# Optimization experiments

Hardware: AMD Instinct MI355X
Metric: run time of the kernel (lower is better)

Reference implementation:

```python
import jax, jax.numpy as jnp
import numpy as np

B, D, H, W = 32, 256, 32, 32
K = 1024
BETA = 0.25


def setup_inputs() -> dict:
    key = jax.random.key(0)
    k1, k2 = jax.random.split(key)
    z_e = jax.random.normal(k1, (B, D, H, W), dtype=jnp.float32)
    codebook_weight = jax.random.normal(k2, (K, D), dtype=jnp.float32)
    return {"z_e": z_e, "codebook_weight": codebook_weight}


def reference(z_e, codebook_weight):
    # NCHW -> NHWC, flatten to tokens [N, D]
    z_perm = jnp.transpose(z_e, (0, 2, 3, 1))            # [B, H, W, D]
    z_flat = z_perm.reshape(-1, codebook_weight.shape[1])  # [N, D]

    # Squared Euclidean distances (argmin-equivalent to torch.cdist argmin)
    # d2[n, k] = ||z_n||^2 - 2 z_n . c_k + ||c_k||^2
    d2 = (jnp.sum(z_flat * z_flat, axis=1, keepdims=True)
          - 2.0 * (z_flat @ codebook_weight.T)
          + jnp.sum(codebook_weight * codebook_weight, axis=1)[None, :])  # [N, K]
    codebook_idx = jnp.argmin(d2, axis=1)                 # [N]

    # one-hot @ codebook == gather
    z_quant = codebook_weight[codebook_idx].reshape(z_perm.shape)  # [B,H,W,D]

    # straight-through estimator, back to NCHW
    z_q = z_perm + jax.lax.stop_gradient(z_quant - z_perm)
    z_q = jnp.transpose(z_q, (0, 3, 1, 2))                # [B, D, H, W]

    loss_codebook = jnp.mean((z_quant - jax.lax.stop_gradient(z_perm)) ** 2)
    loss_commit = jnp.mean((jax.lax.stop_gradient(z_quant) - z_perm) ** 2)
    loss_vq = loss_codebook + loss_commit * BETA

    return z_q, codebook_idx[:, None], loss_vq
```

## Files before the change

### kernel.cpp

```cpp
#include <hip/hip_runtime.h>
#include <hip/hip_bf16.h>
#include <cstdint>

#define B_ 32
#define D_ 256
#define K_ 1024
#define N_TOK 32768
#define Z_ELEMS 8388608
#define OUT_IDX_OFF Z_ELEMS
#define OUT_LOSS_OFF (Z_ELEMS + N_TOK)

#define WS_CNORM_OFF 0
#define WS_PART_OFF  4096
#define WS_CBF_OFF   8192
#define WS_TOP2_OFF  532480

#define MARGIN 1.25f

typedef __attribute__((ext_vector_type(8))) short short8v;
typedef __attribute__((ext_vector_type(4))) float f32x4;
typedef unsigned long long u64;

__device__ __forceinline__ unsigned short f2bf(float x) {
    unsigned u = __float_as_uint(x);
    return (unsigned short)((u + 0x7fffu + ((u >> 16) & 1u)) >> 16);
}
__device__ __forceinline__ unsigned packf(float f) {
    unsigned u = __float_as_uint(f);
    return (u & 0x80000000u) ? ~u : (u | 0x80000000u);
}
__device__ __forceinline__ float unpackf(unsigned p) {
    unsigned u = (p & 0x80000000u) ? (p & 0x7fffffffu) : ~p;
    return __uint_as_float(u);
}
__device__ __forceinline__ void gload16(const void* g, void* l) {
    __builtin_amdgcn_global_load_lds(
        (const __attribute__((address_space(1))) unsigned int*)g,
        (__attribute__((address_space(3))) unsigned int*)l, 16, 0, 0);
}

__global__ __launch_bounds__(256)
void prep_kernel(const float* __restrict__ cb, float* __restrict__ cnorm,
                 unsigned char* __restrict__ cbf) {
    const int t = threadIdx.x;
    const int blk = blockIdx.x;
    {
        int k = blk * 64 + (t >> 2);
        int part = t & 3;
        const float4* row = reinterpret_cast<const float4*>(cb + k * D_);
        float s = 0.f;
#pragma unroll
        for (int j = 0; j < 16; ++j) {
            float4 v = row[part * 16 + j];
            s += v.x * v.x + v.y * v.y + v.z * v.z + v.w * v.w;
        }
        s += __shfl_xor(s, 1);
        s += __shfl_xor(s, 2);
        if (part == 0) cnorm[k] = s;
    }
#pragma unroll
    for (int w = 0; w < 8; ++w) {
        int g = blk * 2048 + w * 256 + t;
        int lane = g & 63, ct = (g >> 6) & 7, kc = (g >> 9) & 7, cblk = g >> 12;
        int code = cblk * 128 + ct * 16 + (lane & 15);
        int d0 = kc * 32 + (lane >> 4) * 8;
        const float* src = cb + code * 256 + d0;
        float4 a = *reinterpret_cast<const float4*>(src);
        float4 b2 = *reinterpret_cast<const float4*>(src + 4);
        uint4 pk;
        pk.x = (unsigned)f2bf(a.x) | ((unsigned)f2bf(a.y) << 16);
        pk.y = (unsigned)f2bf(a.z) | ((unsigned)f2bf(a.w) << 16);
        pk.z = (unsigned)f2bf(b2.x) | ((unsigned)f2bf(b2.y) << 16);
        pk.w = (unsigned)f2bf(b2.z) | ((unsigned)f2bf(b2.w) << 16);
        *reinterpret_cast<uint4*>(cbf + (size_t)g * 16) = pk;
    }
}

__global__ __launch_bounds__(256)
void mm_kernel(const float* __restrict__ z, const unsigned char* __restrict__ cbf,
               const float* __restrict__ cnorm, unsigned* __restrict__ top2) {
    __shared__ __align__(16) unsigned char zfB[32768];
    __shared__ __align__(16) unsigned char Abuf[16384];
    __shared__ float cns[1024];

    const int t = threadIdx.x;
    const int lane = t & 63;
    const int wv = t >> 6;
    const int blk = blockIdx.x;
    const int b = blk >> 4;
    const int hw0 = (blk & 15) << 6;
    const float* zb = z + ((size_t)b << 18) + hw0;

    {
        const unsigned char* g = cbf + (size_t)(wv * 2) * 1024 + lane * 16;
        unsigned char* l = Abuf + (wv * 2) * 1024;
        gload16(g, l);
        gload16(g + 1024, l + 1024);
    }

    for (int i = t; i < 1024; i += 256) cns[i] = cnorm[i];

    {
        const int tok = t & 63;
        const int dseg = t >> 6;
#pragma unroll
        for (int u = 0; u < 8; ++u) {
            int d0 = dseg * 64 + u * 8;
            float v[8];
#pragma unroll
            for (int j = 0; j < 8; ++j) v[j] = zb[(size_t)(d0 + j) * 1024 + tok];
            uint4 pk;
            pk.x = (unsigned)f2bf(v[0]) | ((unsigned)f2bf(v[1]) << 16);
            pk.y = (unsigned)f2bf(v[2]) | ((unsigned)f2bf(v[3]) << 16);
            pk.z = (unsigned)f2bf(v[4]) | ((unsigned)f2bf(v[5]) << 16);
            pk.w = (unsigned)f2bf(v[6]) | ((unsigned)f2bf(v[7]) << 16);
            int kc = d0 >> 5;
            *reinterpret_cast<uint4*>(zfB + (kc * 4 + (tok >> 4)) * 1024 +
                                      ((u & 3) * 16 + (tok & 15)) * 16) = pk;
        }
    }
    __syncthreads();

    const int rbase = (lane >> 4) << 2;

    for (int cblk = 0; cblk < 8; ++cblk) {
        f32x4 acc[8];
#pragma unroll
        for (int mt = 0; mt < 8; ++mt) acc[mt] = (f32x4){0.f, 0.f, 0.f, 0.f};

        for (int kc = 0; kc < 8; ++kc) {
            const int s = cblk * 8 + kc;
            if (s < 63) {
                const unsigned char* g =
                    cbf + (size_t)(s + 1) * 8192 + (wv * 2) * 1024 + lane * 16;
                unsigned char* l = Abuf + ((s + 1) & 1) * 8192 + (wv * 2) * 1024;
                gload16(g, l);
                gload16(g + 1024, l + 1024);
            }
            const unsigned char* ab = Abuf + (s & 1) * 8192 + lane * 16;
            short8v bfv = *reinterpret_cast<const short8v*>(
                zfB + (kc * 4 + wv) * 1024 + lane * 16);
#pragma unroll
            for (int mt = 0; mt < 8; ++mt) {
                short8v af = *reinterpret_cast<const short8v*>(ab + mt * 1024);
                acc[mt] = __builtin_amdgcn_mfma_f32_16x16x32_bf16(af, bfv, acc[mt], 0, 0, 0);
            }
            if (kc == 7) {
                unsigned k1 = 0xFFFFFFFFu, k2 = 0xFFFFFFFFu;
#pragma unroll
                for (int mt = 0; mt < 8; ++mt) {
#pragma unroll
                    for (int r = 0; r < 4; ++r) {
                        int code = cblk * 128 + mt * 16 + rbase + r;
                        float d2a = fmaf(-2.0f, acc[mt][r], cns[code]);
                        unsigned key = (packf(d2a) & 0xFFFFFC00u) | (unsigned)code;
                        if (key < k1) { k2 = k1; k1 = key; }
                        else if (key < k2) { k2 = key; }
                    }
                }
#pragma unroll
                for (int x = 16; x <= 32; x <<= 1) {
                    unsigned o1 = __shfl_xor(k1, x);
                    unsigned o2 = __shfl_xor(k2, x);
                    unsigned n1, n2;
                    if (k1 < o1) { n1 = k1; n2 = (k2 < o1) ? k2 : o1; }
                    else         { n1 = o1; n2 = (o2 < k1) ? o2 : k1; }
                    k1 = n1; k2 = n2;
                }
                if (lane < 16) {
                    int token = blk * 64 + wv * 16 + lane;
                    *reinterpret_cast<uint2*>(top2 + ((size_t)cblk * N_TOK + token) * 2) =
                        make_uint2(k1, k2);
                }
            }
            __syncthreads();
        }
    }
}

__global__ __launch_bounds__(256)
void refgather_kernel(const float* __restrict__ z, const float* __restrict__ cb,
                      const float* __restrict__ cnorm, const unsigned* __restrict__ top2,
                      float* __restrict__ out, float* __restrict__ partials) {
    __shared__ float zsm[32][261];
    __shared__ float crows[32][257];
    __shared__ int cand[32][16];
    __shared__ int cnt[32];
    __shared__ u64 bestk[32];
    __shared__ int sidx[32];
    __shared__ float red[256];
    __shared__ int maxc;

    const int t = threadIdx.x;
    const int bh = blockIdx.x;
    const int b = bh >> 5, h = bh & 31;
    const int n0 = b * 1024 + h * 32;
    const int w = t & 31, dg = t >> 5;

    {
        const float* zp = z + ((size_t)b << 18) + h * 32 + w;
#pragma unroll
        for (int i = 0; i < 32; ++i) {
            int d = dg * 32 + i;
            zsm[w][d] = zp[(size_t)d * 1024];
        }
    }
    if (t < 32) cnt[t] = 0;
    if (t == 0) maxc = 0;
    __syncthreads();

    const int tk = t >> 3, l8 = t & 7;
    {
        uint2 kk = *reinterpret_cast<const uint2*>(
            top2 + ((size_t)l8 * N_TOK + (n0 + tk)) * 2);
        unsigned mn = kk.x;
#pragma unroll
        for (int x = 1; x < 8; x <<= 1) {
            unsigned o = __shfl_xor(mn, x);
            if (o < mn) mn = o;
        }
        float thr = unpackf(mn & 0xFFFFFC00u) + MARGIN;
        float da = unpackf(kk.x & 0xFFFFFC00u);
        if (da <= thr) { int p = atomicAdd(&cnt[tk], 1); cand[tk][p] = (int)(kk.x & 1023u); }
        float db = unpackf(kk.y & 0xFFFFFC00u);
        if (db <= thr) { int p = atomicAdd(&cnt[tk], 1); cand[tk][p] = (int)(kk.y & 1023u); }
    }
    __syncthreads();
    if (t < 32) atomicMax(&maxc, cnt[t]);
    __syncthreads();

    const int mc = maxc;
    u64 best = ~0ull;
    for (int ci = 0; ci < mc; ++ci) {
        if (ci < cnt[tk]) {
            int k = cand[tk][ci];
            const float* crow = cb + (size_t)k * 256;
            float s = 0.f;
#pragma unroll
            for (int j = 0; j < 32; ++j) {
                int d = j * 8 + l8;
                s = fmaf(zsm[tk][d], crow[d], s);
            }
#pragma unroll
            for (int x = 1; x < 8; x <<= 1) s += __shfl_xor(s, x);
            float d2 = cnorm[k] - 2.f * s;
            u64 key = ((u64)packf(d2) << 32) | (unsigned)k;
            if (key < best) best = key;
        }
    }
    if (l8 == 0) bestk[tk] = best;
    __syncthreads();
    if (t < 32) {
        int k = (int)(bestk[t] & 1023ull);
        sidx[t] = k;
        out[OUT_IDX_OFF + n0 + t] = (float)k;
    }
    __syncthreads();
    {
        const int r = t & 31, q = t >> 5;
        const float4* src = reinterpret_cast<const float4*>(cb + (size_t)sidx[r] * 256 + q * 32);
#pragma unroll
        for (int j = 0; j < 8; ++j) {
            float4 v = src[j];
            int d = q * 32 + j * 4;
            crows[r][d] = v.x; crows[r][d + 1] = v.y;
            crows[r][d + 2] = v.z; crows[r][d + 3] = v.w;
        }
    }
    __syncthreads();
    float accl = 0.f;
    float* orow = out + ((size_t)b << 18) + h * 32 + w;
#pragma unroll
    for (int i = 0; i < 32; ++i) {
        const int d = dg * 32 + i;
        const float cv = crows[w][d];
        const float zv = zsm[w][d];
        orow[(size_t)d * 1024] = cv;
        const float df = cv - zv;
        accl += df * df;
    }
    red[t] = accl;
    __syncthreads();
    for (int s = 128; s > 0; s >>= 1) {
        if (t < s) red[t] += red[t + s];
        __syncthreads();
    }
    if (t == 0) partials[bh] = red[0];
}

__global__ __launch_bounds__(256) void loss_kernel(const float* __restrict__ partials,
                                                   float* __restrict__ out) {
    __shared__ float red[256];
    const int t = threadIdx.x;
    float s = partials[t] + partials[t + 256] + partials[t + 512] + partials[t + 768];
    red[t] = s;
    __syncthreads();
    for (int st = 128; st > 0; st >>= 1) {
        if (t < st) red[t] += red[t + st];
        __syncthreads();
    }
    if (t == 0) out[OUT_LOSS_OFF] = red[0] * (1.25f / (float)Z_ELEMS);
}

extern "C" void kernel_launch(void* const* d_in, const int* in_sizes, int n_in,
                              void* d_out, int out_size, void* d_ws, size_t ws_size,
                              hipStream_t stream) {
    const float* z = (const float*)d_in[0];
    const float* cb = (const float*)d_in[1];
    float* out = (float*)d_out;
    float* cnorm = (float*)((char*)d_ws + WS_CNORM_OFF);
    float* partials = (float*)((char*)d_ws + WS_PART_OFF);
    unsigned char* cbf = (unsigned char*)d_ws + WS_CBF_OFF;
    unsigned* top2 = (unsigned*)((char*)d_ws + WS_TOP2_OFF);

    prep_kernel<<<16, 256, 0, stream>>>(cb, cnorm, cbf);
    mm_kernel<<<512, 256, 0, stream>>>(z, cbf, cnorm, top2);
    refgather_kernel<<<1024, 256, 0, stream>>>(z, cb, cnorm, top2, out, partials);
    loss_kernel<<<1, 256, 0, stream>>>(partials, out);
}
```

Baseline: 84.75 us.

## Triple-buffer codebook tiles in mm_kernel and widen prep kernel grid

The matmul kernel moves from double-buffered to triple-buffered LDS staging of bf16 codebook tiles, prefetching two steps ahead. It replaces per-step __syncthreads with a raw s_barrier plus explicit vmcnt waits and sched barriers, and flattens the cblk/kc loops into one macro-expanded step loop with a peeled tail. The aim is to hide global-to-LDS latency and cut synchronisation stalls. Separately, the prep kernel spreads over 64 blocks instead of 16 to parallelise codebook norm and bf16 packing. The hand-counted vmcnt waits rely on a barrier placed before the wait, so one wave may read LDS tiles that another wave has not finished loading. Interleaved top2 stores also add to the counter, which makes the counting harder to trust.

```diff
diff --git a/kernel.cpp b/kernel.cpp
--- a/kernel.cpp
+++ b/kernel.cpp
@@ -45,22 +45,24 @@
     const int t = threadIdx.x;
     const int blk = blockIdx.x;
     {
-        int k = blk * 64 + (t >> 2);
-        int part = t & 3;
+        int k = blk * 16 + (t >> 4);
+        int part = t & 15;
         const float4* row = reinterpret_cast<const float4*>(cb + k * D_);
         float s = 0.f;
 #pragma unroll
-        for (int j = 0; j < 16; ++j) {
-            float4 v = row[part * 16 + j];
+        for (int j = 0; j < 4; ++j) {
+            float4 v = row[part * 4 + j];
             s += v.x * v.x + v.y * v.y + v.z * v.z + v.w * v.w;
         }
         s += __shfl_xor(s, 1);
         s += __shfl_xor(s, 2);
+        s += __shfl_xor(s, 4);
+        s += __shfl_xor(s, 8);
         if (part == 0) cnorm[k] = s;
     }
 #pragma unroll
-    for (int w = 0; w < 8; ++w) {
-        int g = blk * 2048 + w * 256 + t;
+    for (int w = 0; w < 2; ++w) {
+        int g = blk * 512 + w * 256 + t;
         int lane = g & 63, ct = (g >> 6) & 7, kc = (g >> 9) & 7, cblk = g >> 12;
         int code = cblk * 128 + ct * 16 + (lane & 15);
         int d0 = kc * 32 + (lane >> 4) * 8;
@@ -80,7 +82,7 @@
 void mm_kernel(const float* __restrict__ z, const unsigned char* __restrict__ cbf,
                const float* __restrict__ cnorm, unsigned* __restrict__ top2) {
     __shared__ __align__(16) unsigned char zfB[32768];
-    __shared__ __align__(16) unsigned char Abuf[16384];
+    __shared__ __align__(16) unsigned char Abuf[3][8192];
     __shared__ float cns[1024];
 
     const int t = threadIdx.x;
@@ -92,10 +94,12 @@
     const float* zb = z + ((size_t)b << 18) + hw0;
 
     {
-        const unsigned char* g = cbf + (size_t)(wv * 2) * 1024 + lane * 16;
-        unsigned char* l = Abuf + (wv * 2) * 1024;
-        gload16(g, l);
-        gload16(g + 1024, l + 1024);
+        const unsigned char* g0 = cbf + wv * 2048 + lane * 16;
+        gload16(g0, Abuf[0] + wv * 2048);
+        gload16(g0 + 1024, Abuf[0] + wv * 2048 + 1024);
+        const unsigned char* g1 = g0 + 8192;
+        gload16(g1, Abuf[1] + wv * 2048);
+        gload16(g1 + 1024, Abuf[1] + wv * 2048 + 1024);
     }
 
     for (int i = t; i < 1024; i += 256) cns[i] = cnorm[i];
@@ -122,60 +126,74 @@
     __syncthreads();
 
     const int rbase = (lane >> 4) << 2;
-
-    for (int cblk = 0; cblk < 8; ++cblk) {
-        f32x4 acc[8];
-#pragma unroll
-        for (int mt = 0; mt < 8; ++mt) acc[mt] = (f32x4){0.f, 0.f, 0.f, 0.f};
-
-        for (int kc = 0; kc < 8; ++kc) {
-            const int s = cblk * 8 + kc;
-            if (s < 63) {
-                const unsigned char* g =
-                    cbf + (size_t)(s + 1) * 8192 + (wv * 2) * 1024 + lane * 16;
-                unsigned char* l = Abuf + ((s + 1) & 1) * 8192 + (wv * 2) * 1024;
-                gload16(g, l);
-                gload16(g + 1024, l + 1024);
-            }
-            const unsigned char* ab = Abuf + (s & 1) * 8192 + lane * 16;
-            short8v bfv = *reinterpret_cast<const short8v*>(
-                zfB + (kc * 4 + wv) * 1024 + lane * 16);
-#pragma unroll
-            for (int mt = 0; mt < 8; ++mt) {
-                short8v af = *reinterpret_cast<const short8v*>(ab + mt * 1024);
-                acc[mt] = __builtin_amdgcn_mfma_f32_16x16x32_bf16(af, bfv, acc[mt], 0, 0, 0);
-            }
-            if (kc == 7) {
-                unsigned k1 = 0xFFFFFFFFu, k2 = 0xFFFFFFFFu;
-#pragma unroll
-                for (int mt = 0; mt < 8; ++mt) {
-#pragma unroll
-                    for (int r = 0; r < 4; ++r) {
-                        int code = cblk * 128 + mt * 16 + rbase + r;
-                        float d2a = fmaf(-2.0f, acc[mt][r], cns[code]);
-                        unsigned key = (packf(d2a) & 0xFFFFFC00u) | (unsigned)code;
-                        if (key < k1) { k2 = k1; k1 = key; }
-                        else if (key < k2) { k2 = key; }
-                    }
-                }
-#pragma unroll
-                for (int x = 16; x <= 32; x <<= 1) {
-                    unsigned o1 = __shfl_xor(k1, x);
-                    unsigned o2 = __shfl_xor(k2, x);
-                    unsigned n1, n2;
-                    if (k1 < o1) { n1 = k1; n2 = (k2 < o1) ? k2 : o1; }
-                    else         { n1 = o1; n2 = (o2 < k1) ? o2 : k1; }
-                    k1 = n1; k2 = n2;
-                }
-                if (lane < 16) {
-                    int token = blk * 64 + wv * 16 + lane;
-                    *reinterpret_cast<uint2*>(top2 + ((size_t)cblk * N_TOK + token) * 2) =
-                        make_uint2(k1, k2);
-                }
-            }
-            __syncthreads();
-        }
-    }
+    f32x4 acc[8];
+
+#define STEP_BODY(S)                                                                   \
+    do {                                                                               \
+        const int cblk_ = (S) >> 3, kc_ = (S) & 7;                                     \
+        if (kc_ == 0) {                                                                \
+            _Pragma("unroll")                                                          \
+            for (int mt = 0; mt < 8; ++mt) acc[mt] = (f32x4){0.f, 0.f, 0.f, 0.f};      \
+        }                                                                              \
+        const unsigned char* ab = Abuf[(S) % 3] + lane * 16;                           \
+        short8v bfv = *reinterpret_cast<const short8v*>(                               \
+            zfB + (kc_ * 4 + wv) * 1024 + lane * 16);                                  \
+        _Pragma("unroll")                                                              \
+        for (int mt = 0; mt < 8; ++mt) {                                               \
+            short8v af = *reinterpret_cast<const short8v*>(ab + mt * 1024);            \
+            acc[mt] = __builtin_amdgcn_mfma_f32_16x16x32_bf16(af, bfv, acc[mt], 0, 0, 0); \
+        }                                                                              \
+        if (kc_ == 7) {                                                                \
+            unsigned k1 = 0xFFFFFFFFu, k2 = 0xFFFFFFFFu;                               \
+            _Pragma("unroll")                                                          \
+            for (int mt = 0; mt < 8; ++mt) {                                           \
+                _Pragma("unroll")                                                      \
+                for (int r = 0; r < 4; ++r) {                                          \
+                    int code = cblk_ * 128 + mt * 16 + rbase + r;                      \
+                    float d2a = fmaf(-2.0f, acc[mt][r], cns[code]);                    \
+                    unsigned key = (packf(d2a) & 0xFFFFFC00u) | (unsigned)code;        \
+                    if (key < k1) { k2 = k1; k1 = key; }                               \
+                    else if (key < k2) { k2 = key; }                                   \
+                }                                                                      \
+            }                                                                          \
+            _Pragma("unroll")                                                          \
+            for (int x = 16; x <= 32; x <<= 1) {                                       \
+                unsigned o1 = __shfl_xor(k1, x);                                       \
+                unsigned o2 = __shfl_xor(k2, x);                                       \
+                unsigned n1, n2;                                                       \
+                if (k1 < o1) { n1 = k1; n2 = (k2 < o1) ? k2 : o1; }                    \
+                else         { n1 = o1; n2 = (o2 < k1) ? o2 : k1; }                    \
+                k1 = n1; k2 = n2;                                                      \
+            }                                                                          \
+            if (lane < 16) {                                                           \
+                int token = blk * 64 + wv * 16 + lane;                                 \
+                *reinterpret_cast<uint2*>(top2 + ((size_t)cblk_ * N_TOK + token) * 2) = \
+                    make_uint2(k1, k2);                                                \
+            }                                                                          \
+        }                                                                              \
+    } while (0)
+
+    for (int s = 0; s < 62; ++s) {
+        __builtin_amdgcn_s_barrier();
+        {
+            const unsigned char* g = cbf + (size_t)(s + 2) * 8192 + wv * 2048 + lane * 16;
+            unsigned char* l = Abuf[(s + 2) % 3] + wv * 2048;
+            gload16(g, l);
+            gload16(g + 1024, l + 1024);
+        }
+        asm volatile("s_waitcnt vmcnt(4)" ::: "memory");
+        __builtin_amdgcn_sched_barrier(0);
+        STEP_BODY(s);
+    }
+    __builtin_amdgcn_s_barrier();
+    asm volatile("s_waitcnt vmcnt(2)" ::: "memory");
+    __builtin_amdgcn_sched_barrier(0);
+    STEP_BODY(62);
+    __builtin_amdgcn_s_barrier();
+    asm volatile("s_waitcnt vmcnt(0)" ::: "memory");
+    __builtin_amdgcn_sched_barrier(0);
+    STEP_BODY(63);
+#undef STEP_BODY
 }
 
 __global__ __launch_bounds__(256)
@@ -313,7 +331,7 @@
     unsigned char* cbf = (unsigned char*)d_ws + WS_CBF_OFF;
     unsigned* top2 = (unsigned*)((char*)d_ws + WS_TOP2_OFF);
 
-    prep_kernel<<<16, 256, 0, stream>>>(cb, cnorm, cbf);
+    prep_kernel<<<64, 256, 0, stream>>>(cb, cnorm, cbf);
     mm_kernel<<<512, 256, 0, stream>>>(z, cbf, cnorm, top2);
     refgather_kernel<<<1024, 256, 0, stream>>>(z, cb, cnorm, top2, out, partials);
     loss_kernel<<<1, 256, 0, stream>>>(partials, out);
```

New measurement: 86.37 us. Within noise of the previous version (+1.9%).
